# Kernel optimization log

Hardware: AMD Instinct MI355X
Metric: run time of the kernel (lower is better)

The kernel has to match this reference:

```python
import jax, jax.numpy as jnp
import numpy as np
from jax import lax

# Topology constants (windowed DAG: compute node i, at global index N_IN+i,
# reads the FANIN immediately preceding global node values).
N_IN = 16      # number of input nodes
FANIN = 16     # connections per compute node
N_NODES = 512  # topologically ordered compute nodes (hidden + output)
N_OUT = 64     # last N_OUT nodes in node_order are outputs
BATCH = 32768
T = N_IN + N_NODES  # total node count


def setup_inputs() -> dict:
    key = jax.random.key(0)
    k1, k2, k3, k4 = jax.random.split(key, 4)
    x = jax.random.normal(k1, (BATCH, N_IN), dtype=jnp.float32)
    # weights scaled down so tanh is not fully saturated through 512 layers
    weights = jax.random.normal(k2, (N_NODES, FANIN), dtype=jnp.float32) * 0.25
    biases = jax.random.normal(k3, (N_NODES,), dtype=jnp.float32) * 0.1
    responses = 1.0 + 0.1 * jax.random.normal(k4, (N_NODES,), dtype=jnp.float32)
    # src indices for node i: global indices [i, i+FANIN) (== previous FANIN nodes,
    # since N_IN == FANIN). Shape [N_NODES, FANIN], int32, all in [0, T).
    src_idx = (jnp.arange(N_NODES, dtype=jnp.int32)[:, None]
               + jnp.arange(FANIN, dtype=jnp.int32)[None, :]
               + (N_IN - FANIN))
    return {"x": x, "weights": weights, "biases": biases,
            "responses": responses, "src_idx": src_idx}


def _forward(x, weights, biases, responses, src_idx):
    B = x.shape[0]
    # values buffer [B, T]: inputs first, then compute nodes in topo order
    values0 = jnp.zeros((B, T), dtype=x.dtype).at[:, :N_IN].set(x)

    def body(values, xs):
        i, idx_row, w, b, r = xs
        src_vals = jnp.take(values, idx_row, axis=1)        # [B, FANIN] gather
        agg = src_vals @ w                                   # [B] weighted sum
        out = jnp.tanh(agg + b) * r                          # activation
        values = lax.dynamic_update_slice(values, out[:, None], (0, N_IN + i))
        return values, None

    ii = jnp.arange(N_NODES, dtype=jnp.int32)
    values, _ = lax.scan(body, values0, (ii, src_idx, weights, biases, responses))
    return values[:, T - N_OUT:]  # [B, N_OUT]


def reference(x, weights, biases, responses, src_idx):
    return _forward(x, weights, biases, responses, src_idx)
```

## Files before the change

### kernel.cpp

```cpp
#include <hip/hip_runtime.h>


typedef float v4f __attribute__((ext_vector_type(4)));

constexpr int kNOut     = 64;
constexpr int kBatch    = 32768;
constexpr int kQStrideF = 80;
constexpr int kLdsFloats = (128 + 3) * kQStrideF;
constexpr float kScale  = 2.8853900817779268f;

#define QPERM(X, CTRL) __int_as_float(__builtin_amdgcn_update_dpp(            \
    __float_as_int(X), __float_as_int(X), (CTRL), 0xF, 0xF, false))

#define PREFQ(S) {                                                            \
    asm volatile(                                                             \
      "ds_read_b128 %0, %5 offset:0\n\t"                                      \
      "ds_read_b128 %1, %5 offset:64\n\t"                                     \
      "ds_read_b128 %2, %5 offset:128\n\t"                                    \
      "ds_read_b128 %3, %5 offset:192\n\t"                                    \
      "ds_read_b128 %4, %5 offset:256"                                        \
      : "=&v"(qw0[S]), "=&v"(qw1[S]), "=&v"(qw2[S]), "=&v"(qw3[S]),           \
        "=&v"(qb[S])                                                          \
      : "v"(a));                                                              \
    a += kQStrideF * 4; }

#define WAITQ(S)                                                              \
    asm volatile("s_waitcnt lgkmcnt(15)"                                      \
      : "+v"(qw0[S]), "+v"(qw1[S]), "+v"(qw2[S]), "+v"(qw3[S]), "+v"(qb[S]));

#define NODE1(QW, INIV, WA, WB, WC, WD) {                                     \
    float wmask = is_l3 ? 0.0f : (QW).w;             \
    float w15b  = QPERM((QW).w, 0xFF);             \
    float p = fmaf((WA), (QW).x, (INIV));                                     \
    p = fmaf((WB), (QW).y, p);                                                \
    p = fmaf((WC), (QW).z, p);                                                \
    p = fmaf((WD), wmask, p);                                                 \
    float s1 = p + QPERM(p, 0xB1);                   \
    float sf = s1 + QPERM(s1, 0x4E);                 \
    float mg = QPERM((WA), 0x39);                    \
    float acc = fmaf(u_prev, w15b, sf);                \
    float ex  = __builtin_amdgcn_exp2f(acc);                                  \
    float un  = __builtin_amdgcn_rcpf(ex + 1.0f);                             \
    u_prev = un;                                                              \
    (WA) = is_l3 ? un : mg; }

#define NODEQ(S) {                                                            \
    PREFQ(((S) + 3) & 3)                                                      \
    WAITQ(S)                                                                  \
    v4f f0 = qw0[S], f1 = qw1[S], f2 = qw2[S], f3 = qw3[S], fb = qb[S];       \
    NODE1(f0, fb.x, r0, r1, r2, r3)                                           \
    NODE1(f1, fb.y, r1, r2, r3, r0)                                           \
    NODE1(f2, fb.z, r2, r3, r0, r1)                                           \
    NODE1(f3, fb.w, r3, r0, r1, r2) }

__global__ __launch_bounds__(512) void neat_fwd(
    const float* __restrict__ x,
    const float* __restrict__ w,
    const float* __restrict__ bias,
    const float* __restrict__ resp,
    float* __restrict__ out)
{
    __shared__ alignas(16) float ldsw[kLdsFloats];
    __shared__ float rst[512];
    __shared__ float sums[512];

    const int t  = threadIdx.x;
    const int jl = t & 3;
    const bool is_l3 = (jl == 3);

    rst[t] = resp[t];
    __syncthreads();

    const float4* __restrict__ w4 = reinterpret_cast<const float4*>(w);
    #pragma unroll
    for (int k = 0; k < 4; ++k) {
        int i4 = t + k * 512;
        float4 v = w4[i4];
        int n = i4 >> 2, k4 = i4 & 3;
        int s0 = n + 4 * k4;
        float rho0 = (s0 + 0 < 16) ? 1.0f : rst[s0 - 16];
        float rho1 = (s0 + 1 < 16) ? 1.0f : rst[s0 - 15];
        float rho2 = (s0 + 2 < 16) ? 1.0f : rst[s0 - 14];
        float rho3 = (s0 + 3 < 16) ? 1.0f : rst[s0 - 13];
        float wr0 = v.x * rho0, wr1 = v.y * rho1,
              wr2 = v.z * rho2, wr3 = v.w * rho3;
        float ps = (wr0 + wr1) + (wr2 + wr3);
        ps += QPERM(ps, 0xB1);
        ps += QPERM(ps, 0x4E);
        if (jl == 0) sums[n] = ps;
        const float m2k = -2.0f * kScale;
        float4 sc = make_float4(wr0 * m2k, wr1 * m2k, wr2 * m2k, wr3 * m2k);
        *reinterpret_cast<float4*>(
            &ldsw[(n >> 2) * kQStrideF + (n & 3) * 16 + k4 * 4]) = sc;
    }
    __syncthreads();

    {
        float Bq = (bias[t] + sums[t]) * (kScale * 0.25f);
        int q = t >> 2, s = t & 3;
        #pragma unroll
        for (int rep = 0; rep < 4; ++rep)
            ldsw[q * kQStrideF + 64 + rep * 4 + s] = Bq;
    }

    const int e = blockIdx.x * 128 + (t >> 2);
    const float4 xi = reinterpret_cast<const float4*>(x)[e * 4 + jl];
    float r0 = fmaf(-0.5f, xi.x, 0.5f);
    float r1 = fmaf(-0.5f, xi.y, 0.5f);
    float r2 = fmaf(-0.5f, xi.z, 0.5f);
    float r3 = fmaf(-0.5f, xi.w, 0.5f);

    const float4* __restrict__ rr4 = reinterpret_cast<const float4*>(resp);
    const float4 rv0 = rr4[112 + jl], rv1 = rr4[116 + jl],
                 rv2 = rr4[120 + jl], rv3 = rr4[124 + jl];

    float* __restrict__ op = out + (size_t)e * kNOut + jl * 4;

    float u_prev = QPERM(r3, 0xFF);

    __syncthreads();

    unsigned int a = (unsigned int)(unsigned long long)(&ldsw[0])
                   + (unsigned int)(jl << 4);

    v4f qw0[4], qw1[4], qw2[4], qw3[4], qb[4];
    PREFQ(0) PREFQ(1) PREFQ(2)

    #pragma unroll 1
    for (int g = 0; g < 32; ++g) {
        NODEQ(0) NODEQ(1) NODEQ(2) NODEQ(3)
        if (g >= 28) {
            float4 rv = (g == 28) ? rv0 : (g == 29) ? rv1
                      : (g == 30) ? rv2 : rv3;
            float t0 = fmaf(-2.0f, r0, 1.0f);
            float t1 = fmaf(-2.0f, r1, 1.0f);
            float t2 = fmaf(-2.0f, r2, 1.0f);
            float t3 = fmaf(-2.0f, r3, 1.0f);
            *reinterpret_cast<float4*>(op + (g - 28) * 16) =
                make_float4(t0 * rv.x, t1 * rv.y, t2 * rv.z, t3 * rv.w);
        }
    }

    asm volatile("s_waitcnt lgkmcnt(0)" ::: "memory");
}

extern "C" void kernel_launch(void* const* d_in, const int* in_sizes, int n_in,
                              void* d_out, int out_size, void* d_ws, size_t ws_size,
                              hipStream_t stream) {
    const float* x    = (const float*)d_in[0];
    const float* w    = (const float*)d_in[1];
    const float* bias = (const float*)d_in[2];
    const float* resp = (const float*)d_in[3];
    float* out = (float*)d_out;
    dim3 block(512);
    dim3 grid((kBatch * 4) / 512);
    hipLaunchKernelGGL(neat_fwd, grid, block, 0, stream, x, w, bias, resp, out);
}
```

Baseline: 103.0 us.

## Map each batch element to two lanes with eight window values each

```diff
diff --git a/kernel.cpp b/kernel.cpp
--- a/kernel.cpp
+++ b/kernel.cpp
@@ -2,58 +2,56 @@
 
 
 typedef float v4f __attribute__((ext_vector_type(4)));
+typedef float v2f __attribute__((ext_vector_type(2)));
 
 constexpr int kNOut     = 64;
 constexpr int kBatch    = 32768;
-constexpr int kQStrideF = 80;
-constexpr int kLdsFloats = (128 + 3) * kQStrideF;
+constexpr int kGStrideF = 48;
+constexpr int kLdsFloats = (256 + 3) * kGStrideF;
 constexpr float kScale  = 2.8853900817779268f;
 
 #define QPERM(X, CTRL) __int_as_float(__builtin_amdgcn_update_dpp(            \
     __float_as_int(X), __float_as_int(X), (CTRL), 0xF, 0xF, false))
 
-#define PREFQ(S) {                                                            \
+#define PREF(S) {                                                             \
     asm volatile(                                                             \
       "ds_read_b128 %0, %5 offset:0\n\t"                                      \
-      "ds_read_b128 %1, %5 offset:64\n\t"                                     \
-      "ds_read_b128 %2, %5 offset:128\n\t"                                    \
-      "ds_read_b128 %3, %5 offset:192\n\t"                                    \
-      "ds_read_b128 %4, %5 offset:256"                                        \
-      : "=&v"(qw0[S]), "=&v"(qw1[S]), "=&v"(qw2[S]), "=&v"(qw3[S]),           \
-        "=&v"(qb[S])                                                          \
+      "ds_read_b128 %1, %5 offset:16\n\t"                                     \
+      "ds_read_b128 %2, %5 offset:64\n\t"                                     \
+      "ds_read_b128 %3, %5 offset:80\n\t"                                     \
+      "ds_read_b64  %4, %5 offset:128"                                        \
+      : "=&v"(qa[S]), "=&v"(qb[S]), "=&v"(qc[S]), "=&v"(qd[S]), "=&v"(qm[S])  \
       : "v"(a));                                                              \
-    a += kQStrideF * 4; }
+    a += kGStrideF * 4; }
 
-#define WAITQ(S)                                                              \
+#define WAITG(S)                                                              \
     asm volatile("s_waitcnt lgkmcnt(15)"                                      \
-      : "+v"(qw0[S]), "+v"(qw1[S]), "+v"(qw2[S]), "+v"(qw3[S]), "+v"(qb[S]));
+      : "+v"(qa[S]), "+v"(qb[S]), "+v"(qc[S]), "+v"(qd[S]), "+v"(qm[S]));
 
-#define NODE1(QW, INIV, WA, WB, WC, WD) {                                     \
-    float wmask = is_l3 ? 0.0f : (QW).w;             \
-    float w15b  = QPERM((QW).w, 0xFF);             \
-    float p = fmaf((WA), (QW).x, (INIV));                                     \
-    p = fmaf((WB), (QW).y, p);                                                \
-    p = fmaf((WC), (QW).z, p);                                                \
-    p = fmaf((WD), wmask, p);                                                 \
-    float s1 = p + QPERM(p, 0xB1);                   \
-    float sf = s1 + QPERM(s1, 0x4E);                 \
-    float mg = QPERM((WA), 0x39);                    \
-    float acc = fmaf(u_prev, w15b, sf);                \
-    float ex  = __builtin_amdgcn_exp2f(acc);                                  \
-    float un  = __builtin_amdgcn_rcpf(ex + 1.0f);                             \
-    u_prev = un;                                                              \
-    (WA) = is_l3 ? un : mg; }
+#define NODE1(WLO, WHI, BH, W0,W1,W2,W3,W4,W5,W6,W7) {                        \
+    float p = fmaf((W0), (WLO).x, (BH));                                      \
+    p = fmaf((W1), (WLO).y, p);                                               \
+    p = fmaf((W2), (WLO).z, p);                                               \
+    p = fmaf((W3), (WLO).w, p);                                               \
+    p = fmaf((W4), (WHI).x, p);                                               \
+    p = fmaf((W5), (WHI).y, p);                                               \
+    p = fmaf((W6), (WHI).z, p);                                               \
+    p = fmaf((W7), (WHI).w, p);                                               \
+    float sf = p + QPERM(p, 0xB1);                   \
+    float ex = __builtin_amdgcn_exp2f(sf);                                    \
+    float un = __builtin_amdgcn_rcpf(ex + 1.0f);                              \
+    float mg = QPERM((W0), 0xB1);                      \
+    (W0) = is_l1 ? un : mg; }
 
-#define NODEQ(S) {                                                            \
-    PREFQ(((S) + 3) & 3)                                                      \
-    WAITQ(S)                                                                  \
-    v4f f0 = qw0[S], f1 = qw1[S], f2 = qw2[S], f3 = qw3[S], fb = qb[S];       \
-    NODE1(f0, fb.x, r0, r1, r2, r3)                                           \
-    NODE1(f1, fb.y, r1, r2, r3, r0)                                           \
-    NODE1(f2, fb.z, r2, r3, r0, r1)                                           \
-    NODE1(f3, fb.w, r3, r0, r1, r2) }
+#define GROUP(G, O0,O1,O2,O3,O4,O5,O6,O7, P0,P1,P2,P3,P4,P5,P6,P7) {          \
+    PREF(((G) + 3) & 3)                                                       \
+    WAITG((G) & 3)                                                            \
+    NODE1(qa[(G) & 3], qb[(G) & 3], qm[(G) & 3].x,                            \
+          O0,O1,O2,O3,O4,O5,O6,O7)                                            \
+    NODE1(qc[(G) & 3], qd[(G) & 3], qm[(G) & 3].y,                            \
+          P0,P1,P2,P3,P4,P5,P6,P7) }
 
-__global__ __launch_bounds__(512) void neat_fwd(
+__global__ __launch_bounds__(256) void neat_fwd(
     const float* __restrict__ x,
     const float* __restrict__ w,
     const float* __restrict__ bias,
@@ -65,16 +63,17 @@
     __shared__ float sums[512];
 
     const int t  = threadIdx.x;
-    const int jl = t & 3;
-    const bool is_l3 = (jl == 3);
+    const int jl = t & 1;
+    const bool is_l1 = (jl == 1);
 
     rst[t] = resp[t];
+    rst[t + 256] = resp[t + 256];
     __syncthreads();
 
     const float4* __restrict__ w4 = reinterpret_cast<const float4*>(w);
     #pragma unroll
-    for (int k = 0; k < 4; ++k) {
-        int i4 = t + k * 512;
+    for (int k = 0; k < 8; ++k) {
+        int i4 = t + k * 256;
         float4 v = w4[i4];
         int n = i4 >> 2, k4 = i4 & 3;
         int s0 = n + 4 * k4;
@@ -87,57 +86,71 @@
         float ps = (wr0 + wr1) + (wr2 + wr3);
         ps += QPERM(ps, 0xB1);
         ps += QPERM(ps, 0x4E);
-        if (jl == 0) sums[n] = ps;
+        if ((t & 3) == 0) sums[n] = ps;
         const float m2k = -2.0f * kScale;
         float4 sc = make_float4(wr0 * m2k, wr1 * m2k, wr2 * m2k, wr3 * m2k);
         *reinterpret_cast<float4*>(
-            &ldsw[(n >> 2) * kQStrideF + (n & 3) * 16 + k4 * 4]) = sc;
+            &ldsw[(n >> 1) * kGStrideF + (n & 1) * 16 + k4 * 4]) = sc;
     }
     __syncthreads();
 
-    {
-        float Bq = (bias[t] + sums[t]) * (kScale * 0.25f);
-        int q = t >> 2, s = t & 3;
-        #pragma unroll
-        for (int rep = 0; rep < 4; ++rep)
-            ldsw[q * kQStrideF + 64 + rep * 4 + s] = Bq;
+    #pragma unroll
+    for (int k = 0; k < 2; ++k) {
+        int n = t + k * 256;
+        float Bh = (bias[n] + sums[n]) * (kScale * 0.5f);
+        int q = n >> 1, s = n & 1;
+        ldsw[q * kGStrideF + 32 + s] = Bh;
+        ldsw[q * kGStrideF + 40 + s] = Bh;
     }
 
-    const int e = blockIdx.x * 128 + (t >> 2);
-    const float4 xi = reinterpret_cast<const float4*>(x)[e * 4 + jl];
-    float r0 = fmaf(-0.5f, xi.x, 0.5f);
-    float r1 = fmaf(-0.5f, xi.y, 0.5f);
-    float r2 = fmaf(-0.5f, xi.z, 0.5f);
-    float r3 = fmaf(-0.5f, xi.w, 0.5f);
+    const int e = blockIdx.x * 128 + (t >> 1);
+    const float4 xa = reinterpret_cast<const float4*>(x)[e * 4 + 2 * jl];
+    const float4 xb = reinterpret_cast<const float4*>(x)[e * 4 + 2 * jl + 1];
+    float r0 = fmaf(-0.5f, xa.x, 0.5f);
+    float r1 = fmaf(-0.5f, xa.y, 0.5f);
+    float r2 = fmaf(-0.5f, xa.z, 0.5f);
+    float r3 = fmaf(-0.5f, xa.w, 0.5f);
+    float r4 = fmaf(-0.5f, xb.x, 0.5f);
+    float r5 = fmaf(-0.5f, xb.y, 0.5f);
+    float r6 = fmaf(-0.5f, xb.z, 0.5f);
+    float r7 = fmaf(-0.5f, xb.w, 0.5f);
 
     const float4* __restrict__ rr4 = reinterpret_cast<const float4*>(resp);
-    const float4 rv0 = rr4[112 + jl], rv1 = rr4[116 + jl],
-                 rv2 = rr4[120 + jl], rv3 = rr4[124 + jl];
-
-    float* __restrict__ op = out + (size_t)e * kNOut + jl * 4;
-
-    float u_prev = QPERM(r3, 0xFF);
+    float* __restrict__ op = out + (size_t)e * kNOut + jl * 8;
 
     __syncthreads();
 
     unsigned int a = (unsigned int)(unsigned long long)(&ldsw[0])
-                   + (unsigned int)(jl << 4);
+                   + (unsigned int)(jl << 5);
 
-    v4f qw0[4], qw1[4], qw2[4], qw3[4], qb[4];
-    PREFQ(0) PREFQ(1) PREFQ(2)
+    v4f qa[4], qb[4], qc[4], qd[4];
+    v2f qm[4];
+    PREF(0) PREF(1) PREF(2)
 
     #pragma unroll 1
     for (int g = 0; g < 32; ++g) {
-        NODEQ(0) NODEQ(1) NODEQ(2) NODEQ(3)
+        GROUP(0, r0,r1,r2,r3,r4,r5,r6,r7,  r1,r2,r3,r4,r5,r6,r7,r0)
+        GROUP(1, r2,r3,r4,r5,r6,r7,r0,r1,  r3,r4,r5,r6,r7,r0,r1,r2)
+        GROUP(2, r4,r5,r6,r7,r0,r1,r2,r3,  r5,r6,r7,r0,r1,r2,r3,r4)
+        GROUP(3, r6,r7,r0,r1,r2,r3,r4,r5,  r7,r0,r1,r2,r3,r4,r5,r6)
+        GROUP(4, r0,r1,r2,r3,r4,r5,r6,r7,  r1,r2,r3,r4,r5,r6,r7,r0)
+        GROUP(5, r2,r3,r4,r5,r6,r7,r0,r1,  r3,r4,r5,r6,r7,r0,r1,r2)
+        GROUP(6, r4,r5,r6,r7,r0,r1,r2,r3,  r5,r6,r7,r0,r1,r2,r3,r4)
+        GROUP(7, r6,r7,r0,r1,r2,r3,r4,r5,  r7,r0,r1,r2,r3,r4,r5,r6)
         if (g >= 28) {
-            float4 rv = (g == 28) ? rv0 : (g == 29) ? rv1
-                      : (g == 30) ? rv2 : rv3;
-            float t0 = fmaf(-2.0f, r0, 1.0f);
-            float t1 = fmaf(-2.0f, r1, 1.0f);
-            float t2 = fmaf(-2.0f, r2, 1.0f);
-            float t3 = fmaf(-2.0f, r3, 1.0f);
-            *reinterpret_cast<float4*>(op + (g - 28) * 16) =
-                make_float4(t0 * rv.x, t1 * rv.y, t2 * rv.z, t3 * rv.w);
+            int m = g - 28;
+            const float4 ra = rr4[112 + 4 * m + 2 * jl];
+            const float4 rb = rr4[112 + 4 * m + 2 * jl + 1];
+            float4 o0 = make_float4(fmaf(-2.0f, r0, 1.0f) * ra.x,
+                                    fmaf(-2.0f, r1, 1.0f) * ra.y,
+                                    fmaf(-2.0f, r2, 1.0f) * ra.z,
+                                    fmaf(-2.0f, r3, 1.0f) * ra.w);
+            float4 o1 = make_float4(fmaf(-2.0f, r4, 1.0f) * rb.x,
+                                    fmaf(-2.0f, r5, 1.0f) * rb.y,
+                                    fmaf(-2.0f, r6, 1.0f) * rb.z,
+                                    fmaf(-2.0f, r7, 1.0f) * rb.w);
+            *reinterpret_cast<float4*>(op + 16 * m)     = o0;
+            *reinterpret_cast<float4*>(op + 16 * m + 4) = o1;
         }
     }
 
@@ -152,7 +165,7 @@
     const float* bias = (const float*)d_in[2];
     const float* resp = (const float*)d_in[3];
     float* out = (float*)d_out;
-    dim3 block(512);
-    dim3 grid((kBatch * 4) / 512);
+    dim3 block(256);
+    dim3 grid(kBatch / 128);
     hipLaunchKernelGGL(neat_fwd, grid, block, 0, stream, x, w, bias, resp, out);
 }
```

After: 89.35 us. -13.3%, faster.
